# Optimization experiments

Hardware: AMD Instinct MI355X
Metric: run time of the kernel (lower is better)

## Reference

```python
import jax, jax.numpy as jnp
import numpy as np

SMOOTH = 1.0      # self.smooth
NUM_ITER = 10     # iter_
EPS = 1e-07
INF = 1e12        # stand-in for +inf in squared-distance init


def _maxpool(x, window):
    # torch max_pool3d(stride=1, padding=w//2): pad with -inf, window max
    pads = ((0, 0), (0, 0)) + tuple((w // 2, w // 2) for w in window)
    return jax.lax.reduce_window(x, -jnp.inf, jax.lax.max, (1, 1) + window, (1, 1, 1, 1, 1), pads)


def _soft_erode(x):  # x: [B,1,D,H,W]
    p1 = -_maxpool(-x, (3, 1, 1))
    p2 = -_maxpool(-x, (1, 3, 1))
    p3 = -_maxpool(-x, (1, 1, 3))
    return jnp.minimum(jnp.minimum(p1, p2), p3)


def _soft_open(x):
    return _maxpool(_soft_erode(x), (3, 3, 3))  # dilate(erode(x))


def _soft_skel(x, n_iter):
    skel = jax.nn.relu(x - _soft_open(x))
    for _ in range(n_iter):
        x = _soft_erode(x)
        delta = jax.nn.relu(x - _soft_open(x))
        skel = skel + jax.nn.relu(delta - skel * delta)
    return skel


def _edt_pass(d2, axis):
    # 1D squared-distance min-convolution: out[i] = min_j (i-j)^2 + d2[j]
    L = d2.shape[axis]
    d2m = jnp.moveaxis(d2, axis, -1)                 # [..., L]
    i = jnp.arange(L, dtype=d2.dtype)
    sq = (i[:, None] - i[None, :]) ** 2              # [L, L]
    out = jnp.min(d2m[..., None, :] + sq, axis=-1)   # [..., L]
    return jnp.moveaxis(out, -1, axis)


def _edt(mask):
    # exact Euclidean distance transform: distance of nonzero voxels to nearest zero voxel
    d2 = jnp.where(mask > 0, INF, 0.0).astype(jnp.float32)  # [B,D,H,W]
    for ax in (1, 2, 3):
        d2 = _edt_pass(d2, ax)
    return jnp.sqrt(d2)


def _get_weights(mask, skel):
    # mask, skel: [B,D,H,W] binary float
    dist = _edt(mask)
    dist = jnp.where(mask == 0, 0.0, dist)
    on_skel = skel == 1
    skel_r = jnp.where(on_skel, dist, 0.0)
    rmax = jnp.max(skel_r.reshape(skel_r.shape[0], -1), axis=1).reshape(-1, 1, 1, 1)
    valid = rmax > 0
    rmax_safe = jnp.where(valid, rmax, 1.0)
    dist_n = jnp.where(valid, dist / rmax_safe, dist)
    skel_rn = jnp.where(valid, skel_r / rmax_safe, skel_r)
    # dim == 3 branch: skel_1_R2_norm
    skel_1r2 = jnp.where(on_skel, (1.0 + EPS) / (skel_rn ** 2 + EPS), 0.0)
    return dist_n, skel_rn, skel_1r2


def _combine(A, B, C):
    # D = B*C, overwritten by A*C where (A != 0) & (B == 0)
    return jnp.where((A != 0) & (B == 0), A * C, B * C)


def reference(y_pred, y_true):
    # y_pred: [B,C,D,H,W] logits; y_true: [B,1,D,H,W] int labels
    fore = jnp.max(y_pred[:, 1:], axis=1, keepdims=True)
    logits = jnp.concatenate([y_pred[:, :1], fore], axis=1)   # [B,2,D,H,W]
    prob = jax.nn.softmax(logits, axis=1)
    yp = (prob[:, 1] > 0.5).astype(jnp.float32)               # [B,D,H,W]
    yt = (y_true > 0).astype(jnp.float32)[:, 0]               # [B,D,H,W]

    skel_p = _soft_skel(yp[:, None], NUM_ITER)[:, 0]
    skel_t = _soft_skel(yt[:, None], NUM_ITER)[:, 0]

    q_vl, q_slvl, q_sl = _get_weights(yt, skel_t)
    q_vp, q_spvp, q_sp = _get_weights(yp, skel_p)

    w_tprec = (jnp.sum(q_sp * q_vl) + SMOOTH) / (jnp.sum(_combine(q_spvp, q_slvl, q_sp)) + SMOOTH)
    w_tsens = (jnp.sum(q_sl * q_vp) + SMOOTH) / (jnp.sum(_combine(q_slvl, q_spvp, q_sl)) + SMOOTH)
    return 1.0 - 2.0 * (w_tprec * w_tsens) / (w_tprec + w_tsens)


def setup_inputs() -> dict:
    key = jax.random.key(0)
    k1, k2 = jax.random.split(key)
    y_pred = jax.random.normal(k1, (2, 2, 64, 96, 96), dtype=jnp.float32)
    y_true = jax.random.randint(k2, (2, 1, 64, 96, 96), 0, 2, dtype=jnp.int32)
    return {"y_pred": y_pred, "y_true": y_true}
```

## Files before the change

kernel.cpp:

```cpp
#include <hip/hip_runtime.h>

namespace {

constexpr int Bn = 2;
constexpr int Dn = 64;
constexpr int Hn = 96;
constexpr int Wn = 96;
constexpr int HW = Hn * Wn;
constexpr int S  = Dn * HW;
constexpr int NBS = Bn * S;
constexpr int NT  = 2 * NBS;
constexpr int WPR = Wn / 32;
constexpr int WPP = HW / 32;
constexpr int WPS = S / 32;
constexpr int NTW = NT / 32;
constexpr float INFD = 1e12f;
constexpr float EPSf = 1e-7f;
constexpr int BLK_SUMS = NBS / 4 / 256;

__global__ __launch_bounds__(256) void k_bin_edt0(const float* __restrict__ logits,
                                                  const int* __restrict__ labels,
                                                  unsigned* __restrict__ Mb,
                                                  float* __restrict__ D2) {
  __shared__ unsigned bits[64];
  int slab = blockIdx.x / 288;
  int cg = blockIdx.x - slab * 288;
  int c0 = cg * 32;
  int tid = threadIdx.x;
  int lane = tid & 63;
  for (int t = tid; t < 2048; t += 256) {
    int zz = t >> 5;
    int col = t & 31;
    int s = zz * HW + c0 + col;
    bool v;
    if (slab < 2) {
      float l0 = logits[(slab * 2 + 0) * S + s];
      float l1 = logits[(slab * 2 + 1) * S + s];
      v = l1 > l0;
    } else {
      v = labels[(slab - 2) * S + s] > 0;
    }
    unsigned long long m = __ballot(v);
    if (lane == 0) {
      unsigned w = (unsigned)m;
      bits[zz] = w;
      Mb[slab * WPS + zz * WPP + cg] = w;
    } else if (lane == 32) {
      unsigned w = (unsigned)(m >> 32);
      bits[zz] = w;
      Mb[slab * WPS + zz * WPP + cg] = w;
    }
  }
  __syncthreads();
  int col = tid & 31;
  int chunk = tid >> 5;
  int i0 = chunk * 8;
  float best[8];
  #pragma unroll
  for (int s = 0; s < 8; ++s) best[s] = 3.4e38f;
  float db = (float)i0;
  #pragma unroll 4
  for (int j = 0; j < Dn; ++j) {
    float f = ((bits[j] >> col) & 1u) ? INFD : 0.0f;
    #pragma unroll
    for (int s = 0; s < 8; ++s) {
      float d = db + (float)s;
      best[s] = fminf(best[s], fmaf(d, d, f));
    }
    db -= 1.0f;
  }
  float* o = D2 + slab * S + c0 + col;
  #pragma unroll
  for (int s = 0; s < 8; ++s) o[(i0 + s) * HW] = best[s];
}

__global__ __launch_bounds__(256) void k_skel11(const unsigned* __restrict__ x,
                                                unsigned* __restrict__ skel) {
  __shared__ unsigned bufA[3600];
  __shared__ unsigned bufB[3174];
  __shared__ unsigned Sbuf[72];
  int slab = blockIdx.x >> 8;
  int z = (blockIdx.x >> 2) & 63;
  int y0 = (blockIdx.x & 3) * 24;
  int tid = threadIdx.x;
  const unsigned* xs = x + slab * WPS;
  for (int t = tid; t < 25 * 48 * 3; t += 256) {
    int p = t / 144;
    int rem = t - p * 144;
    int r = rem / 3;
    int wx = rem - r * 3;
    int zz = z - 12 + p, yy = y0 - 12 + r;
    bufA[t] = (zz >= 0 && zz < Dn && yy >= 0 && yy < Hn)
                ? xs[zz * WPP + yy * WPR + wx] : 0xFFFFFFFFu;
  }
  __syncthreads();
  unsigned skreg = 0u;
  int ro = tid / 3, wxo = tid - ro * 3;
  int yyo = y0 + ro;
  #pragma unroll
  for (int k = 1; k <= 11; ++k) {
    unsigned* src = (k & 1) ? bufA : bufB;
    unsigned* dst = (k & 1) ? bufB : bufA;
    const int Rs = 50 - 2 * k;
    const int Pd = 25 - 2 * k, Rd = 48 - 2 * k;
    const int ps = Rs * 3;
    for (int t = tid; t < Pd * Rd * 3; t += 256) {
      int p = t / (Rd * 3);
      int rem = t - p * (Rd * 3);
      int r = rem / 3;
      int wx = rem - r * 3;
      int ci = ((p + 1) * Rs + (r + 1)) * 3 + wx;
      unsigned v = src[ci];
      unsigned l = (v << 1) | (wx > 0 ? (src[ci - 1] >> 31) : 1u);
      unsigned rr = (v >> 1) | (wx < 2 ? (src[ci + 1] << 31) : 0x80000000u);
      dst[t] = v & l & rr & src[ci - 3] & src[ci + 3] & src[ci - ps] & src[ci + ps];
    }
    __syncthreads();
    if (tid < 72) {
      const int pc = 12 - k;
      const int rb = ro + 12 - k;
      unsigned s = 0u;
      #pragma unroll
      for (int dz = -1; dz <= 1; ++dz) {
        if (z + dz < 0 || z + dz >= Dn) continue;
        #pragma unroll
        for (int dy = -1; dy <= 1; ++dy) {
          if (yyo + dy < 0 || yyo + dy >= Hn) continue;
          s |= dst[((pc + dz) * Rd + (rb + dy)) * 3 + wxo];
        }
      }
      Sbuf[tid] = s;
    }
    __syncthreads();
    if (tid < 72) {
      unsigned s = Sbuf[tid];
      unsigned pw = (wxo > 0) ? Sbuf[tid - 1] : 0u;
      unsigned nw = (wxo < 2) ? Sbuf[tid + 1] : 0u;
      unsigned acc = s | ((s << 1) | (pw >> 31)) | ((s >> 1) | (nw << 31));
      unsigned prevC = src[((13 - k) * Rs + (ro + 13 - k)) * 3 + wxo];
      skreg |= prevC & ~acc;
    }
    __syncthreads();
  }
  if (tid < 72) {
    int gi = slab * WPS + z * WPP + yyo * WPR + wxo;
    skel[gi] = skreg;
  }
}

__global__ __launch_bounds__(192) void k_edt12(const float* __restrict__ D2,
                                               float* __restrict__ EF,
                                               const unsigned* __restrict__ skel,
                                               float* __restrict__ pmax) {
  __shared__ float Bh[24 * 97];
  __shared__ float ldsf[3];
  int slab = blockIdx.x >> 8;
  int zz = (blockIdx.x >> 2) & 63;
  int y0 = (blockIdx.x & 3) * 24;
  int tid = threadIdx.x;
  int pb = slab * S + zz * HW;
  {
    int xx = tid % 96;
    int c = tid / 96;
    float best[12];
    #pragma unroll
    for (int s = 0; s < 12; ++s) best[s] = 3.4e38f;
    float db = (float)(y0 + c * 12);
    #pragma unroll 4
    for (int j = 0; j < Hn; ++j) {
      float f = D2[pb + j * 96 + xx];
      #pragma unroll
      for (int s = 0; s < 12; ++s) {
        float d = db + (float)s;
        best[s] = fminf(best[s], fmaf(d, d, f));
      }
      db -= 1.0f;
    }
    #pragma unroll
    for (int s = 0; s < 12; ++s) Bh[(c * 12 + s) * 97 + xx] = best[s];
  }
  __syncthreads();
  float m = 0.0f;
  {
    int r = tid >> 3;
    int chunk = tid & 7;
    int i0 = chunk * 12;
    float best[12];
    #pragma unroll
    for (int s = 0; s < 12; ++s) best[s] = 3.4e38f;
    float db = (float)i0;
    #pragma unroll 4
    for (int j = 0; j < Wn; ++j) {
      float f = Bh[r * 97 + j];
      #pragma unroll
      for (int s = 0; s < 12; ++s) {
        float d = db + (float)s;
        best[s] = fminf(best[s], fmaf(d, d, f));
      }
      db -= 1.0f;
    }
    int gb = pb + (y0 + r) * 96 + i0;
    ((float4*)(EF + gb))[0] = make_float4(best[0], best[1], best[2], best[3]);
    ((float4*)(EF + gb))[1] = make_float4(best[4], best[5], best[6], best[7]);
    ((float4*)(EF + gb))[2] = make_float4(best[8], best[9], best[10], best[11]);
    int sh = gb & 31;
    unsigned w0 = skel[gb >> 5];
    unsigned w1 = (sh + 11 > 31) ? skel[(gb >> 5) + 1] : 0u;
    unsigned long long wv = ((unsigned long long)w1 << 32) | (unsigned long long)w0;
    unsigned bitsv = (unsigned)(wv >> sh);
    #pragma unroll
    for (int s = 0; s < 12; ++s)
      if ((bitsv >> s) & 1u) m = fmaxf(m, best[s]);
  }
  #pragma unroll
  for (int o = 32; o > 0; o >>= 1) m = fmaxf(m, __shfl_xor(m, o, 64));
  if ((tid & 63) == 0) ldsf[tid >> 6] = m;
  __syncthreads();
  if (tid == 0)
    pmax[blockIdx.x] = fmaxf(fmaxf(ldsf[0], ldsf[1]), ldsf[2]);
}

__global__ __launch_bounds__(256) void k_sums(const float* __restrict__ d2,
                                              const unsigned* __restrict__ skel,
                                              const float* __restrict__ pmax,
                                              double* __restrict__ ps) {
  __shared__ float lmax[4];
  __shared__ double ldsd[4][4];
  int tid = threadIdx.x;
  {
    int wave = tid >> 6, lane = tid & 63;
    const float* pw = pmax + wave * 256;
    float v = fmaxf(fmaxf(pw[lane], pw[lane + 64]),
                    fmaxf(pw[lane + 128], pw[lane + 192]));
    #pragma unroll
    for (int o = 32; o > 0; o >>= 1) v = fmaxf(v, __shfl_xor(v, o, 64));
    if (lane == 0) lmax[wave] = v;
  }
  __syncthreads();
  int q = blockIdx.x * 256 + tid;
  int idx0 = q * 4;
  int b = idx0 / S;
  float rmax_p = sqrtf(lmax[b]);
  float rmax_t = sqrtf(lmax[2 + b]);
  float4 dp4 = ((const float4*)d2)[q];
  float4 dt4 = ((const float4*)(d2 + NBS))[q];
  unsigned spw = (skel[idx0 >> 5] >> (idx0 & 31)) & 0xFu;
  unsigned stw = (skel[(NBS + idx0) >> 5] >> (idx0 & 31)) & 0xFu;
  const float* dp = &dp4.x;
  const float* dt = &dt4.x;
  double acc[4] = {0.0, 0.0, 0.0, 0.0};
  #pragma unroll
  for (int s = 0; s < 4; ++s) {
    float dist_p = sqrtf(dp[s]);
    float dist_t = sqrtf(dt[s]);
    bool sp = (spw >> s) & 1u;
    bool st = (stw >> s) & 1u;
    float q_vp = (rmax_p > 0.0f) ? dist_p / rmax_p : dist_p;
    float q_vl = (rmax_t > 0.0f) ? dist_t / rmax_t : dist_t;
    float q_spvp = sp ? q_vp : 0.0f;
    float q_slvl = st ? q_vl : 0.0f;
    float q_sp = sp ? (1.0f + EPSf) / (q_spvp * q_spvp + EPSf) : 0.0f;
    float q_sl = st ? (1.0f + EPSf) / (q_slvl * q_slvl + EPSf) : 0.0f;
    acc[0] += (double)(q_sp * q_vl);
    acc[1] += (double)(((q_spvp != 0.0f) && (q_slvl == 0.0f)) ? q_spvp * q_sp
                                                              : q_slvl * q_sp);
    acc[2] += (double)(q_sl * q_vp);
    acc[3] += (double)(((q_slvl != 0.0f) && (q_spvp == 0.0f)) ? q_slvl * q_sl
                                                              : q_spvp * q_sl);
  }
  #pragma unroll
  for (int k = 0; k < 4; ++k)
    #pragma unroll
    for (int o = 32; o > 0; o >>= 1)
      acc[k] += __shfl_xor(acc[k], o, 64);
  if ((tid & 63) == 0) {
    #pragma unroll
    for (int k = 0; k < 4; ++k) ldsd[tid >> 6][k] = acc[k];
  }
  __syncthreads();
  if (tid == 0) {
    #pragma unroll
    for (int k = 0; k < 4; ++k)
      ps[blockIdx.x * 4 + k] = ldsd[0][k] + ldsd[1][k] + ldsd[2][k] + ldsd[3][k];
  }
}

__global__ __launch_bounds__(256) void k_final(const double* __restrict__ ps,
                                               float* __restrict__ out) {
  __shared__ double ldsd[4][4];
  int tid = threadIdx.x;
  double s[4] = {0.0, 0.0, 0.0, 0.0};
  for (int i = tid; i < BLK_SUMS; i += 256) {
    s[0] += ps[i * 4 + 0];
    s[1] += ps[i * 4 + 1];
    s[2] += ps[i * 4 + 2];
    s[3] += ps[i * 4 + 3];
  }
  #pragma unroll
  for (int k = 0; k < 4; ++k)
    #pragma unroll
    for (int o = 32; o > 0; o >>= 1)
      s[k] += __shfl_xor(s[k], o, 64);
  if ((tid & 63) == 0) {
    #pragma unroll
    for (int k = 0; k < 4; ++k) ldsd[tid >> 6][k] = s[k];
  }
  __syncthreads();
  if (tid == 0) {
    double tot[4];
    #pragma unroll
    for (int k = 0; k < 4; ++k)
      tot[k] = ldsd[0][k] + ldsd[1][k] + ldsd[2][k] + ldsd[3][k];
    double wp = (tot[0] + 1.0) / (tot[1] + 1.0);
    double ws = (tot[2] + 1.0) / (tot[3] + 1.0);
    out[0] = (float)(1.0 - 2.0 * (wp * ws) / (wp + ws));
  }
}

}

extern "C" void kernel_launch(void* const* d_in, const int* in_sizes, int n_in,
                              void* d_out, int out_size, void* d_ws, size_t ws_size,
                              hipStream_t stream) {
  (void)in_sizes; (void)n_in; (void)out_size; (void)ws_size;
  const float* logits = (const float*)d_in[0];
  const int* labels   = (const int*)d_in[1];
  float* out = (float*)d_out;

  float* D2 = (float*)d_ws;
  float* EF = D2 + NT;
  unsigned* MB    = (unsigned*)(EF + NT);
  unsigned* SKELB = MB + NTW;
  float* PMAX  = (float*)(SKELB + NTW);
  double* PS   = (double*)(PMAX + 1024);

  k_bin_edt0<<<1152, 256, 0, stream>>>(logits, labels, MB, D2);
  k_skel11<<<1024, 256, 0, stream>>>(MB, SKELB);
  k_edt12<<<1024, 192, 0, stream>>>(D2, EF, SKELB, PMAX);
  k_sums<<<1152, 256, 0, stream>>>(EF, SKELB, PMAX, PS);
  k_final<<<1, 256, 0, stream>>>(PS, out);
}
```

Measured before the change: 140.8 us.

## Use bit-scan nearest-zero for first EDT pass and expand squares in later passes

The first (depth-axis) distance pass is replaced by a bitmask transpose plus count-leading/trailing-zero scans. Each voxel's nearest zero along depth is found directly, instead of a 64-step min-convolution. The H and W passes expand (i-j)^2+f as i^2 - 2ij + (j^2+f), so the inner loop needs only one FMA and one min per candidate, and i^2 is added at the end. This cuts ALU work in the EDT kernels, but expanding the squares can change float rounding when f is large (1e12), and the unroll factor drops from 4 to 2.

```diff
diff --git a/kernel.cpp b/kernel.cpp
--- a/kernel.cpp
+++ b/kernel.cpp
@@ -14,15 +14,16 @@
 constexpr int WPP = HW / 32;
 constexpr int WPS = S / 32;
 constexpr int NTW = NT / 32;
-constexpr float INFD = 1e12f;
 constexpr float EPSf = 1e-7f;
 constexpr int BLK_SUMS = NBS / 4 / 256;
+#define BIGF 1e12f
 
 __global__ __launch_bounds__(256) void k_bin_edt0(const float* __restrict__ logits,
                                                   const int* __restrict__ labels,
                                                   unsigned* __restrict__ Mb,
                                                   float* __restrict__ D2) {
   __shared__ unsigned bits[64];
+  __shared__ unsigned zlo[32], zhi[32];
   int slab = blockIdx.x / 288;
   int cg = blockIdx.x - slab * 288;
   int c0 = cg * 32;
@@ -52,26 +53,37 @@
     }
   }
   __syncthreads();
+  if (tid < 64) {
+    int col = tid & 31;
+    int base = (tid < 32) ? 0 : 32;
+    unsigned zw = 0u;
+    #pragma unroll
+    for (int j = 0; j < 32; ++j)
+      zw |= (((bits[base + j] >> col) & 1u) ^ 1u) << j;
+    if (tid < 32) zlo[col] = zw; else zhi[col] = zw;
+  }
+  __syncthreads();
   int col = tid & 31;
   int chunk = tid >> 5;
   int i0 = chunk * 8;
-  float best[8];
-  #pragma unroll
-  for (int s = 0; s < 8; ++s) best[s] = 3.4e38f;
-  float db = (float)i0;
-  #pragma unroll 4
-  for (int j = 0; j < Dn; ++j) {
-    float f = ((bits[j] >> col) & 1u) ? INFD : 0.0f;
-    #pragma unroll
-    for (int s = 0; s < 8; ++s) {
-      float d = db + (float)s;
-      best[s] = fminf(best[s], fmaf(d, d, f));
-    }
-    db -= 1.0f;
-  }
+  unsigned long long Z = ((unsigned long long)zhi[col] << 32) | (unsigned long long)zlo[col];
   float* o = D2 + slab * S + c0 + col;
   #pragma unroll
-  for (int s = 0; s < 8; ++s) o[(i0 + s) * HW] = best[s];
+  for (int s = 0; s < 8; ++s) {
+    int i = i0 + s;
+    unsigned long long below = Z & ((2ull << i) - 1ull);
+    unsigned long long above = Z >> i;
+    float outv;
+    if (below | above) {
+      int ddn = below ? (i - (63 - __builtin_clzll(below))) : 99;
+      int dup = above ? __builtin_ctzll(above) : 99;
+      int d = ddn < dup ? ddn : dup;
+      outv = (float)(d * d);
+    } else {
+      outv = BIGF;
+    }
+    o[i * HW] = outv;
+  }
 }
 
 __global__ __launch_bounds__(256) void k_skel11(const unsigned* __restrict__ x,
@@ -162,22 +174,28 @@
   {
     int xx = tid % 96;
     int c = tid / 96;
+    int ybase = y0 + c * 12;
+    float m2[12];
+    #pragma unroll
+    for (int s = 0; s < 12; ++s) m2[s] = -2.0f * (float)(ybase + s);
     float best[12];
     #pragma unroll
     for (int s = 0; s < 12; ++s) best[s] = 3.4e38f;
-    float db = (float)(y0 + c * 12);
-    #pragma unroll 4
+    float jf = 0.0f;
+    #pragma unroll 2
     for (int j = 0; j < Hn; ++j) {
       float f = D2[pb + j * 96 + xx];
+      float g = fmaf(jf, jf, f);
       #pragma unroll
-      for (int s = 0; s < 12; ++s) {
-        float d = db + (float)s;
-        best[s] = fminf(best[s], fmaf(d, d, f));
-      }
-      db -= 1.0f;
-    }
-    #pragma unroll
-    for (int s = 0; s < 12; ++s) Bh[(c * 12 + s) * 97 + xx] = best[s];
+      for (int s = 0; s < 12; ++s)
+        best[s] = fminf(best[s], fmaf(m2[s], jf, g));
+      jf += 1.0f;
+    }
+    #pragma unroll
+    for (int s = 0; s < 12; ++s) {
+      float yf = (float)(ybase + s);
+      Bh[(c * 12 + s) * 97 + xx] = fmaf(yf, yf, best[s]);
+    }
   }
   __syncthreads();
   float m = 0.0f;
@@ -185,24 +203,32 @@
     int r = tid >> 3;
     int chunk = tid & 7;
     int i0 = chunk * 12;
+    float m2[12];
+    #pragma unroll
+    for (int s = 0; s < 12; ++s) m2[s] = -2.0f * (float)(i0 + s);
     float best[12];
     #pragma unroll
     for (int s = 0; s < 12; ++s) best[s] = 3.4e38f;
-    float db = (float)i0;
-    #pragma unroll 4
+    float jf = 0.0f;
+    #pragma unroll 2
     for (int j = 0; j < Wn; ++j) {
       float f = Bh[r * 97 + j];
+      float g = fmaf(jf, jf, f);
       #pragma unroll
-      for (int s = 0; s < 12; ++s) {
-        float d = db + (float)s;
-        best[s] = fminf(best[s], fmaf(d, d, f));
-      }
-      db -= 1.0f;
+      for (int s = 0; s < 12; ++s)
+        best[s] = fminf(best[s], fmaf(m2[s], jf, g));
+      jf += 1.0f;
+    }
+    float outv[12];
+    #pragma unroll
+    for (int s = 0; s < 12; ++s) {
+      float xf = (float)(i0 + s);
+      outv[s] = fmaf(xf, xf, best[s]);
     }
     int gb = pb + (y0 + r) * 96 + i0;
-    ((float4*)(EF + gb))[0] = make_float4(best[0], best[1], best[2], best[3]);
-    ((float4*)(EF + gb))[1] = make_float4(best[4], best[5], best[6], best[7]);
-    ((float4*)(EF + gb))[2] = make_float4(best[8], best[9], best[10], best[11]);
+    ((float4*)(EF + gb))[0] = make_float4(outv[0], outv[1], outv[2], outv[3]);
+    ((float4*)(EF + gb))[1] = make_float4(outv[4], outv[5], outv[6], outv[7]);
+    ((float4*)(EF + gb))[2] = make_float4(outv[8], outv[9], outv[10], outv[11]);
     int sh = gb & 31;
     unsigned w0 = skel[gb >> 5];
     unsigned w1 = (sh + 11 > 31) ? skel[(gb >> 5) + 1] : 0u;
@@ -210,7 +236,7 @@
     unsigned bitsv = (unsigned)(wv >> sh);
     #pragma unroll
     for (int s = 0; s < 12; ++s)
-      if ((bitsv >> s) & 1u) m = fmaxf(m, best[s]);
+      if ((bitsv >> s) & 1u) m = fmaxf(m, outv[s]);
   }
   #pragma unroll
   for (int o = 32; o > 0; o >>= 1) m = fmaxf(m, __shfl_xor(m, o, 64));
```

Result: faster. 136.5 us (-3.1%).
